# Performance work log

Measured on AMD Instinct MI355X. Metric: run time of the kernel, lower is better.

The kernel has to match this reference:

```python
import jax, jax.numpy as jnp
import numpy as np

D, U, H = 3, 256, 8
DH = U // H
B, N, E = 128, 128, 512
BN_SCALE = 1.0 / np.sqrt(1.0 + 1e-3)  # keras BatchNorm inference with init moving stats (mean=0, var=1)


def setup_inputs() -> dict:
    key = jax.random.key(0)
    k = jax.random.split(key, 16)
    p = lambda kk, sh: jax.random.normal(kk, sh, jnp.float32) * 0.05
    return {
        "node_attr": jax.random.normal(k[0], (B, N, U), jnp.float32),
        "edge_attr": jax.random.normal(k[1], (B, E, U), jnp.float32),
        "edge_indices": jax.random.randint(k[2], (B, E, 2), 0, N, dtype=jnp.int32),
        "W_edge": p(k[3], (D, 3 * U, U)), "b_edge": jnp.zeros((D, U)),
        "gamma_e": jnp.ones((D, U)), "beta_e": jnp.zeros((D, U)),
        "W_node": p(k[4], (D, U, U)), "b_node": jnp.zeros((D, U)),
        "gamma_n": jnp.ones((D, U)), "beta_n": jnp.zeros((D, U)),
        "W_gat": p(k[5], (D, U, H, DH)), "a_gat": p(k[6], (D, H, 2 * DH + U)), "b_gat": jnp.zeros((D, H)),
        "W_gru": p(k[7], (D, U, 3 * U)), "U_gru": p(k[8], (D, U, 3 * U)), "b_gru": jnp.zeros((D, 3 * U)),
        "W_p1": p(k[9], (U, U)), "b_p1": jnp.zeros((U,)),
        "W_p2": p(k[10], (U, U // 2)), "b_p2": jnp.zeros((U // 2,)),
    }


def _bn(x, gamma, beta):
    # inference batchnorm with moving_mean=0, moving_var=1
    return x * (gamma * BN_SCALE) + beta


def _gather(nodes, idx):
    # nodes [B,N,F], idx [B,E] -> [B,E,F]
    return jnp.take_along_axis(nodes, idx[..., None], axis=1)


def _gat_one(h, eidx, edge, a, b):
    # h [N,H,DH], eidx [E,2], edge [E,U]; aggregate messages from src (col 1) at tgt (col 0)
    tgt, src = eidx[:, 0], eidx[:, 1]
    hi, hj = h[tgt], h[src]
    logit = (jnp.einsum('ehd,hd->eh', hi, a[:, :DH])
             + jnp.einsum('ehd,hd->eh', hj, a[:, DH:2 * DH])
             + edge @ a[:, 2 * DH:].T + b)
    logit = jax.nn.leaky_relu(logit, 0.2)
    # per-target-node segment softmax over variable-degree neighborhoods
    m = jnp.full((N, H), -1e9, logit.dtype).at[tgt].max(logit)
    ex = jnp.exp(logit - m[tgt])
    den = jnp.zeros((N, H), logit.dtype).at[tgt].add(ex) + 1e-9
    att = ex / den[tgt]
    out = jnp.zeros((N, H, DH), h.dtype).at[tgt].add(att[..., None] * hj)
    return out.reshape(N, H * DH)


def reference(node_attr, edge_attr, edge_indices, W_edge, b_edge, gamma_e, beta_e,
              W_node, b_node, gamma_n, beta_n, W_gat, a_gat, b_gat,
              W_gru, U_gru, b_gru, W_p1, b_p1, W_p2, b_p2):
    nodes, edges = node_attr, edge_attr
    tgt_idx = edge_indices[..., 0]
    src_idx = edge_indices[..., 1]
    for d in range(D):
        # edge update: gather endpoints, concat with edge feats, MLP, graph batchnorm
        e_in = _gather(nodes, src_idx)   # GatherNodesOutgoing
        e_out = _gather(nodes, tgt_idx)  # GatherNodesIngoing
        ec = jnp.concatenate([e_in, e_out, edges], axis=-1)  # [B,E,3U]
        e_up = _bn(jax.nn.relu(ec @ W_edge[d] + b_edge[d]), gamma_e[d], beta_e[d])
        # multi-head GAT attention over edges
        h = jnp.einsum('bnf,fhd->bnhd', nodes, W_gat[d])
        attended = jax.nn.relu(jax.vmap(_gat_one, in_axes=(0, 0, 0, None, None))(
            h, edge_indices, e_up, a_gat[d], b_gat[d]))
        # node MLP + batchnorm
        n_up = _bn(jax.nn.relu(nodes @ W_node[d] + b_node[d]), gamma_n[d], beta_n[d])
        # GRU update: state = n_up, input = attended
        xp = attended @ W_gru[d] + b_gru[d]
        hp = n_up @ U_gru[d]
        z = jax.nn.sigmoid(xp[..., :U] + hp[..., :U])
        r = jax.nn.sigmoid(xp[..., U:2 * U] + hp[..., U:2 * U])
        hh = jnp.tanh(xp[..., 2 * U:] + r * hp[..., 2 * U:])
        nodes = z * n_up + (1.0 - z) * hh
        edges = e_up
    emb = jnp.mean(nodes, axis=1)
    emb = jax.nn.relu(emb @ W_p1 + b_p1)
    emb = jax.nn.relu(emb @ W_p2 + b_p2)
    # inference-mode view augmentation is identity, so both views equal the base embedding
    views = jnp.stack([emb, emb], axis=1)  # [B, num_views, U//2]
    return emb, views
```

## Files before the change

### kernel.cpp

```cpp
#include <hip/hip_runtime.h>
#include <hip/hip_bf16.h>

constexpr int Dn  = 3;
constexpr int Un  = 256;
constexpr int Hn  = 8;
constexpr int DHn = 32;
constexpr int Bn  = 128;
constexpr int Nn  = 128;
constexpr int En  = 512;
constexpr float BN_SCALE_C = 0.9995003746877732f;

#define LB __launch_bounds__(256)
#define LB8 __launch_bounds__(512)

typedef short bf16x8 __attribute__((ext_vector_type(8)));
typedef unsigned short u16x8 __attribute__((ext_vector_type(8)));
typedef float f32x4 __attribute__((ext_vector_type(4)));
#define MFMA16(a, b, c) __builtin_amdgcn_mfma_f32_16x16x32_bf16(a, b, c, 0, 0, 0)

__device__ __forceinline__ void gload16(const void* g, void* l) {
  __builtin_amdgcn_global_load_lds(
      (const __attribute__((address_space(1))) void*)g,
      (__attribute__((address_space(3))) void*)l, 16, 0, 0);
}
__device__ __forceinline__ float sigm(float x) { return 1.f / (1.f + expf(-x)); }
__device__ __forceinline__ float bf2f(unsigned short u) {
  return __uint_as_float((unsigned)u << 16);
}

__global__ LB void k_f2bf(const float* __restrict__ in,
                          __hip_bfloat16* __restrict__ out, int n) {
  int i = (blockIdx.x * 256 + threadIdx.x) * 4;
  if (i + 3 < n) {
    float4 v = *reinterpret_cast<const float4*>(in + i);
    out[i + 0] = __float2bfloat16(v.x);
    out[i + 1] = __float2bfloat16(v.y);
    out[i + 2] = __float2bfloat16(v.z);
    out[i + 3] = __float2bfloat16(v.w);
  }
}

__global__ LB void k_prep_edge(const float* __restrict__ W,
                               __hip_bfloat16* __restrict__ Wt) {
  int idx = blockIdx.x * 256 + threadIdx.x;
  int d = idx / (Un * 3 * Un);
  int rem = idx % (Un * 3 * Un);
  int n = rem / (3 * Un);
  int k = rem % (3 * Un);
  Wt[idx] = __float2bfloat16(W[(size_t)d * 3 * Un * Un + (size_t)k * Un + n]);
}

__global__ LB void k_prep_hn(const float* __restrict__ Wg,
                             const float* __restrict__ Wn,
                             __hip_bfloat16* __restrict__ Wt) {
  int idx = blockIdx.x * 256 + threadIdx.x;
  int d = idx / (512 * 256);
  int rem = idx % (512 * 256);
  int n = rem / 256;
  int k = rem % 256;
  float v = (n < 256) ? Wg[(size_t)d * 65536 + k * 256 + n]
                      : Wn[(size_t)d * 65536 + k * 256 + (n - 256)];
  Wt[idx] = __float2bfloat16(v);
}

__global__ LB void k_prep_gru2(const float* __restrict__ W,
                               const float* __restrict__ U,
                               __hip_bfloat16* __restrict__ Wt) {
  int idx = blockIdx.x * 256 + threadIdx.x;
  int d = idx / (768 * 512);
  int rem = idx % (768 * 512);
  int j2 = rem >> 9;
  int k = rem & 511;
  const size_t wb = (size_t)d * 196608;
  float v = (k < 256) ? W[wb + k * 768 + j2] : U[wb + (k - 256) * 768 + j2];
  Wt[idx] = __float2bfloat16(v);
}

__global__ LB8 void k_edge_mfma(const __hip_bfloat16* __restrict__ nodes,
                                const __hip_bfloat16* __restrict__ edges,
                                const int* __restrict__ eidx,
                                const __hip_bfloat16* __restrict__ Wt,
                                const float* __restrict__ bias,
                                const float* __restrict__ gamma,
                                const float* __restrict__ beta,
                                __hip_bfloat16* __restrict__ e_up) {
  __shared__ __align__(16) short As[128 * 64];
  __shared__ __align__(16) short Bs[256 * 64];
  const int tid = threadIdx.x, lane = tid & 63;
  const int w = tid >> 6, wr = w >> 2, wc = w & 3;
  const int bid = blockIdx.x;
  const int wgid = (bid & 7) * 64 + (bid >> 3);
  const int row0 = wgid * 128;
  const __hip_bfloat16 *pa0[2], *pa1[2], *pa2[2], *pb[4];
  int sxa[2], sxb[4];
#pragma unroll
  for (int i = 0; i < 2; ++i) {
    int c = i * 512 + tid, row = c >> 3, slot = c & 7;
    int R = row0 + row, b = R >> 9, e = R & 511;
    int tt = eidx[(b * En + e) * 2 + 0];
    int ss = eidx[(b * En + e) * 2 + 1];
    pa0[i] = nodes + (size_t)(b * Nn + ss) * Un;
    pa1[i] = nodes + (size_t)(b * Nn + tt) * Un;
    pa2[i] = edges + (size_t)(b * En + e) * Un;
    sxa[i] = (slot ^ (row & 7)) * 8;
  }
#pragma unroll
  for (int i = 0; i < 4; ++i) {
    int c = i * 512 + tid, j = c >> 3, slot = c & 7;
    pb[i] = Wt + (size_t)j * 768;
    sxb[i] = (slot ^ (j & 7)) * 8;
  }
  f32x4 acc[4][4] = {};
  const int ldsb = (tid & 448) * 16;
  for (int kt = 0; kt < 768; kt += 64) {
    const int region = kt >> 8, koff = kt & 255;
#pragma unroll
    for (int i = 0; i < 2; ++i) {
      const __hip_bfloat16* s = (region == 0) ? pa0[i] : (region == 1 ? pa1[i] : pa2[i]);
      gload16(s + koff + sxa[i], (char*)As + i * 8192 + ldsb);
    }
#pragma unroll
    for (int i = 0; i < 4; ++i)
      gload16(pb[i] + kt + sxb[i], (char*)Bs + i * 8192 + ldsb);
    __syncthreads();
#pragma unroll
    for (int ks = 0; ks < 2; ++ks) {
      const int lc = ks * 4 + (lane >> 4);
      bf16x8 af[4], bfv[4];
#pragma unroll
      for (int mi = 0; mi < 4; ++mi) {
        int row = wr * 64 + mi * 16 + (lane & 15);
        af[mi] = *(const bf16x8*)((const char*)As + row * 128 + ((lc ^ (row & 7)) << 4));
      }
#pragma unroll
      for (int ni = 0; ni < 4; ++ni) {
        int col = wc * 64 + ni * 16 + (lane & 15);
        bfv[ni] = *(const bf16x8*)((const char*)Bs + col * 128 + ((lc ^ (col & 7)) << 4));
      }
#pragma unroll
      for (int mi = 0; mi < 4; ++mi)
#pragma unroll
        for (int ni = 0; ni < 4; ++ni)
          acc[mi][ni] = MFMA16(af[mi], bfv[ni], acc[mi][ni]);
    }
    __syncthreads();
  }
#pragma unroll
  for (int mi = 0; mi < 4; ++mi)
#pragma unroll
    for (int ni = 0; ni < 4; ++ni) {
      int C = wc * 64 + ni * 16 + (lane & 15);
      float gs = gamma[C] * BN_SCALE_C, bt = beta[C], bi = bias[C];
#pragma unroll
      for (int r = 0; r < 4; ++r) {
        int R = row0 + wr * 64 + mi * 16 + (lane >> 4) * 4 + r;
        float v = acc[mi][ni][r] + bi;
        v = fmaxf(v, 0.f) * gs + bt;
        e_up[(size_t)R * Un + C] = __float2bfloat16(v);
      }
    }
}

__global__ LB8 void k_hn_mfma(const __hip_bfloat16* __restrict__ A,
                              const __hip_bfloat16* __restrict__ Wt,
                              const float* __restrict__ nb,
                              const float* __restrict__ ng,
                              const float* __restrict__ nbe,
                              __hip_bfloat16* __restrict__ h_bf,
                              __hip_bfloat16* __restrict__ nupb) {
  __shared__ __align__(16) short As[128 * 64];
  __shared__ __align__(16) short Bs[256 * 64];
  const int tid = threadIdx.x, lane = tid & 63;
  const int w = tid >> 6, wr = w >> 2, wc = w & 3;
  const int bid = blockIdx.x;
  const int wgid = (bid & 7) * 32 + (bid >> 3);
  const int row0 = (wgid >> 1) * 128, col0 = (wgid & 1) * 256;
  const __hip_bfloat16 *pa[2], *pb[4];
  int sxa[2], sxb[4];
#pragma unroll
  for (int i = 0; i < 2; ++i) {
    int c = i * 512 + tid, row = c >> 3, slot = c & 7;
    pa[i] = A + (size_t)(row0 + row) * Un;
    sxa[i] = (slot ^ (row & 7)) * 8;
  }
#pragma unroll
  for (int i = 0; i < 4; ++i) {
    int c = i * 512 + tid, j = c >> 3, slot = c & 7;
    pb[i] = Wt + (size_t)(col0 + j) * Un;
    sxb[i] = (slot ^ (j & 7)) * 8;
  }
  f32x4 acc[4][4] = {};
  const int ldsb = (tid & 448) * 16;
  for (int kt = 0; kt < 256; kt += 64) {
#pragma unroll
    for (int i = 0; i < 2; ++i)
      gload16(pa[i] + kt + sxa[i], (char*)As + i * 8192 + ldsb);
#pragma unroll
    for (int i = 0; i < 4; ++i)
      gload16(pb[i] + kt + sxb[i], (char*)Bs + i * 8192 + ldsb);
    __syncthreads();
#pragma unroll
    for (int ks = 0; ks < 2; ++ks) {
      const int lc = ks * 4 + (lane >> 4);
      bf16x8 af[4], bfv[4];
#pragma unroll
      for (int mi = 0; mi < 4; ++mi) {
        int row = wr * 64 + mi * 16 + (lane & 15);
        af[mi] = *(const bf16x8*)((const char*)As + row * 128 + ((lc ^ (row & 7)) << 4));
      }
#pragma unroll
      for (int ni = 0; ni < 4; ++ni) {
        int col = wc * 64 + ni * 16 + (lane & 15);
        bfv[ni] = *(const bf16x8*)((const char*)Bs + col * 128 + ((lc ^ (col & 7)) << 4));
      }
#pragma unroll
      for (int mi = 0; mi < 4; ++mi)
#pragma unroll
        for (int ni = 0; ni < 4; ++ni)
          acc[mi][ni] = MFMA16(af[mi], bfv[ni], acc[mi][ni]);
    }
    __syncthreads();
  }
  const bool is_h = (col0 < 256);
#pragma unroll
  for (int mi = 0; mi < 4; ++mi)
#pragma unroll
    for (int ni = 0; ni < 4; ++ni) {
      int c2 = wc * 64 + ni * 16 + (lane & 15);
#pragma unroll
      for (int r = 0; r < 4; ++r) {
        int R = row0 + wr * 64 + mi * 16 + (lane >> 4) * 4 + r;
        float v = acc[mi][ni][r];
        if (is_h) {
          h_bf[(size_t)R * Un + c2] = __float2bfloat16(v);
        } else {
          v += nb[c2];
          v = fmaxf(v, 0.f) * (ng[c2] * BN_SCALE_C) + nbe[c2];
          nupb[(size_t)R * Un + c2] = __float2bfloat16(v);
        }
      }
    }
}

__global__ LB8 void k_gru_mfma3(const __hip_bfloat16* __restrict__ attb,
                                const __hip_bfloat16* __restrict__ nupb,
                                const __hip_bfloat16* __restrict__ Wt,
                                const float* __restrict__ bg,
                                __hip_bfloat16* __restrict__ nodes_out) {
  __shared__ __align__(16) short As[128 * 64];
  __shared__ __align__(16) short Bs[192 * 64];
  const int tid = threadIdx.x, lane = tid & 63;
  const int w = tid >> 6, wr = w >> 2, wc = w & 3;
  const int bid = blockIdx.x;
  const int wgid = (bid & 7) * 64 + (bid >> 3);
  const int row0 = (wgid >> 2) * 128, c0 = (wgid & 3) * 64;
  const __hip_bfloat16 *paA[2], *paN[2], *pb[3];
  int sxa[2], sxb[3];
#pragma unroll
  for (int i = 0; i < 2; ++i) {
    int c = i * 512 + tid, row = c >> 3, slot = c & 7;
    paA[i] = attb + (size_t)(row0 + row) * Un;
    paN[i] = nupb + (size_t)(row0 + row) * Un;
    sxa[i] = (slot ^ (row & 7)) * 8;
  }
#pragma unroll
  for (int i = 0; i < 3; ++i) {
    int l = i * 512 + tid, j = l >> 3, slot = l & 7;
    int sec = j >> 6, jj = j & 63;
    pb[i] = Wt + (size_t)(sec * 256 + c0 + jj) * 512;
    sxb[i] = (slot ^ (j & 7)) * 8;
  }
  f32x4 acc[4][4] = {};
  const int ldsb = (tid & 448) * 16;
  for (int kt = 0; kt < 512; kt += 64) {
    const int koff = kt & 255;
    const bool rA = kt < 256;
#pragma unroll
    for (int i = 0; i < 2; ++i) {
      const __hip_bfloat16* s = rA ? paA[i] : paN[i];
      gload16(s + koff + sxa[i], (char*)As + i * 8192 + ldsb);
    }
#pragma unroll
    for (int i = 0; i < 3; ++i)
      gload16(pb[i] + kt + sxb[i], (char*)Bs + i * 8192 + ldsb);
    __syncthreads();
    const int g2 = rA ? 2 : 3;
#pragma unroll
    for (int ks = 0; ks < 2; ++ks) {
      const int lc = ks * 4 + (lane >> 4);
      bf16x8 af[4], bv[3];
#pragma unroll
      for (int s = 0; s < 3; ++s) {
        int j = s * 64 + wc * 16 + (lane & 15);
        bv[s] = *(const bf16x8*)((const char*)Bs + j * 128 + ((lc ^ (j & 7)) << 4));
      }
#pragma unroll
      for (int mi = 0; mi < 4; ++mi) {
        int row = wr * 64 + mi * 16 + (lane & 15);
        af[mi] = *(const bf16x8*)((const char*)As + row * 128 + ((lc ^ (row & 7)) << 4));
      }
#pragma unroll
      for (int mi = 0; mi < 4; ++mi) {
        acc[0][mi] = MFMA16(af[mi], bv[0], acc[0][mi]);
        acc[1][mi] = MFMA16(af[mi], bv[1], acc[1][mi]);
        acc[g2][mi] = MFMA16(af[mi], bv[2], acc[g2][mi]);
      }
    }
    __syncthreads();
  }
  {
    const int c = c0 + wc * 16 + (lane & 15);
    const float bz = bg[c], br = bg[256 + c], bh = bg[512 + c];
    const unsigned short* nu_u = (const unsigned short*)nupb;
#pragma unroll
    for (int mi = 0; mi < 4; ++mi)
#pragma unroll
      for (int r = 0; r < 4; ++r) {
        int R = row0 + wr * 64 + mi * 16 + (lane >> 4) * 4 + r;
        float z  = sigm(acc[0][mi][r] + bz);
        float rr = sigm(acc[1][mi][r] + br);
        float hh = tanhf(acc[2][mi][r] + bh + rr * acc[3][mi][r]);
        float nu = bf2f(nu_u[(size_t)R * Un + c]);
        nodes_out[(size_t)R * Un + c] = __float2bfloat16(z * nu + (1.f - z) * hh);
      }
  }
}

__global__ LB void k_elog_mfma(const __hip_bfloat16* __restrict__ e_up,
                               const float* __restrict__ a_gat,
                               float* __restrict__ elog) {
  __shared__ __align__(16) short at[16 * 264];
  const int tid = threadIdx.x, lane = tid & 63, w = tid >> 6;
  for (int l = tid; l < 16 * 264; l += 256) {
    int col = l / 264, k = l % 264;
    float v = (col < 8 && k < 256) ? a_gat[col * 320 + 64 + k] : 0.f;
    __hip_bfloat16 b = __float2bfloat16(v);
    at[l] = *reinterpret_cast<short*>(&b);
  }
  __syncthreads();
  const int rowbase = blockIdx.x * 256 + w * 64;
  const int lrow = lane & 15, lk = (lane >> 4) * 8;
  f32x4 acc[4] = {};
#pragma unroll
  for (int kt = 0; kt < 256; kt += 32) {
    bf16x8 bf = *(const bf16x8*)(at + lrow * 264 + kt + lk);
#pragma unroll
    for (int mi = 0; mi < 4; ++mi) {
      bf16x8 af = *(const bf16x8*)(e_up + (size_t)(rowbase + mi * 16 + lrow) * 256 + kt + lk);
      acc[mi] = MFMA16(af, bf, acc[mi]);
    }
  }
  if (lrow < 8) {
#pragma unroll
    for (int mi = 0; mi < 4; ++mi)
#pragma unroll
      for (int r = 0; r < 4; ++r) {
        int row = rowbase + mi * 16 + (lane >> 4) * 4 + r;
        elog[(size_t)row * 8 + lrow] = acc[mi][r];
      }
  }
}

__global__ LB void k_gat4(const __hip_bfloat16* __restrict__ h,
                          const float* __restrict__ elog,
                          const int* __restrict__ eidx,
                          const float* __restrict__ a_gat,
                          const float* __restrict__ b_gat,
                          __hip_bfloat16* __restrict__ att_bf) {
  const int b = blockIdx.x, q = blockIdx.y;
  __shared__ int s_tgt[En], s_src[En];
  __shared__ float s_at[32], s_as[32];
  __shared__ float s_lt[Nn], s_ls[Nn];
  __shared__ float s_L[En];
  __shared__ int s_cnt[Nn], s_start[Nn], s_cur[Nn];
  __shared__ short s_ord[En];
  __shared__ __align__(16) unsigned short hl[Nn][40];
  const int tid = threadIdx.x;
  const float bgq = b_gat[q];
  if (tid < 32) {
    s_at[tid] = a_gat[q * 320 + tid];
    s_as[tid] = a_gat[q * 320 + 32 + tid];
  }
  for (int e = tid; e < En; e += 256) {
    s_tgt[e] = eidx[(b * En + e) * 2 + 0];
    s_src[e] = eidx[(b * En + e) * 2 + 1];
  }
  if (tid < Nn) s_cnt[tid] = 0;
  for (int e = tid; e < En; e += 256)
    s_L[e] = elog[(size_t)(b * En + e) * 8 + q];
  const unsigned short* hu = (const unsigned short*)h;
  for (int l = tid; l < Nn * 4; l += 256) {
    int row = l >> 2, c8 = l & 3;
    u16x8 v = *(const u16x8*)(hu + (size_t)(b * Nn + row) * Un + q * DHn + c8 * 8);
    *(u16x8*)&hl[row][c8 * 8] = v;
  }
  __syncthreads();
  if (tid < Nn) {
    const unsigned short* hr = hl[tid];
    float lt = 0.f, ls = 0.f;
#pragma unroll
    for (int c8 = 0; c8 < 4; ++c8) {
      u16x8 v = *(const u16x8*)(hr + c8 * 8);
#pragma unroll
      for (int j = 0; j < 8; ++j) {
        float f = bf2f(v[j]);
        int d = c8 * 8 + j;
        lt += f * s_at[d];
        ls += f * s_as[d];
      }
    }
    s_lt[tid] = lt; s_ls[tid] = ls;
  }
  for (int e = tid; e < En; e += 256) atomicAdd(&s_cnt[s_tgt[e]], 1);
  __syncthreads();
  if (tid == 0) {
    int acc = 0;
    for (int n = 0; n < Nn; ++n) { s_start[n] = acc; s_cur[n] = acc; acc += s_cnt[n]; }
  }
  __syncthreads();
  for (int e = tid; e < En; e += 256) {
    int pos = atomicAdd(&s_cur[s_tgt[e]], 1);
    s_ord[pos] = (short)e;
  }
  for (int e = tid; e < En; e += 256) {
    float v = s_lt[s_tgt[e]] + s_ls[s_src[e]] + s_L[e] + bgq;
    v = (v > 0.f) ? v : 0.2f * v;
    s_L[e] = v;
  }
  __syncthreads();
  if (tid < Nn) {
    const int st = s_start[tid], cn = s_cnt[tid];
    float m = -1e9f;
    for (int i = 0; i < cn; ++i) m = fmaxf(m, s_L[s_ord[st + i]]);
    float den = 1e-9f;
    for (int i = 0; i < cn; ++i) {
      const int e = s_ord[st + i];
      float ex = expf(s_L[e] - m);
      s_L[e] = ex;
      den += ex;
    }
    s_lt[tid] = 1.f / den;
  }
  __syncthreads();
  {
    const int n = tid >> 1, half = tid & 1;
    const int st = s_start[n], cn = s_cnt[n];
    const float inv = s_lt[n];
    float acc[16] = {};
    for (int i = 0; i < cn; ++i) {
      const int e = s_ord[st + i];
      const float wgt = s_L[e] * inv;
      const unsigned short* hs = &hl[s_src[e]][half * 16];
#pragma unroll
      for (int c8 = 0; c8 < 2; ++c8) {
        u16x8 v = *(const u16x8*)(hs + c8 * 8);
#pragma unroll
        for (int j = 0; j < 8; ++j) acc[c8 * 8 + j] += wgt * bf2f(v[j]);
      }
    }
    __hip_bfloat16* ob = att_bf + (size_t)(b * Nn + n) * Un + q * DHn + half * 16;
#pragma unroll
    for (int d = 0; d < 16; ++d) ob[d] = __float2bfloat16(fmaxf(acc[d], 0.f));
  }
}

__global__ LB void k_pool(const __hip_bfloat16* __restrict__ nodes,
                          const float* __restrict__ Wp1, const float* __restrict__ bp1,
                          const float* __restrict__ Wp2, const float* __restrict__ bp2,
                          float* __restrict__ out) {
  const int b = blockIdx.x, tid = threadIdx.x;
  __shared__ float e0[256], e1[256];
  float s = 0.f;
  for (int n = 0; n < Nn; ++n) s += __bfloat162float(nodes[(size_t)(b * Nn + n) * Un + tid]);
  e0[tid] = s * (1.f / Nn);
  __syncthreads();
  float a1 = bp1[tid];
  for (int k = 0; k < 256; ++k) a1 += e0[k] * Wp1[k * 256 + tid];
  e1[tid] = fmaxf(a1, 0.f);
  __syncthreads();
  if (tid < 128) {
    float a2 = bp2[tid];
    for (int k = 0; k < 256; ++k) a2 += e1[k] * Wp2[k * 128 + tid];
    a2 = fmaxf(a2, 0.f);
    out[b * 128 + tid] = a2;
    out[Bn * 128 + b * 256 + tid] = a2;
    out[Bn * 128 + b * 256 + 128 + tid] = a2;
  }
}

extern "C" void kernel_launch(void* const* d_in, const int* in_sizes, int n_in,
                              void* d_out, int out_size, void* d_ws, size_t ws_size,
                              hipStream_t stream) {
  const float* node_attr = (const float*)d_in[0];
  const float* edge_attr = (const float*)d_in[1];
  const int*   eidx      = (const int*)d_in[2];
  const float* W_edge    = (const float*)d_in[3];
  const float* b_edge    = (const float*)d_in[4];
  const float* gamma_e   = (const float*)d_in[5];
  const float* beta_e    = (const float*)d_in[6];
  const float* W_node    = (const float*)d_in[7];
  const float* b_node    = (const float*)d_in[8];
  const float* gamma_n   = (const float*)d_in[9];
  const float* beta_n    = (const float*)d_in[10];
  const float* W_gat     = (const float*)d_in[11];
  const float* a_gat     = (const float*)d_in[12];
  const float* b_gat     = (const float*)d_in[13];
  const float* W_gru     = (const float*)d_in[14];
  const float* U_gru     = (const float*)d_in[15];
  const float* b_gru     = (const float*)d_in[16];
  const float* W_p1      = (const float*)d_in[17];
  const float* b_p1      = (const float*)d_in[18];
  const float* W_p2      = (const float*)d_in[19];
  const float* b_p2      = (const float*)d_in[20];

  char* p = (char*)d_ws;
  auto alloc = [&](size_t bytes) { char* q = p; p += (bytes + 255) & ~255ull; return q; };
  const size_t NODE_EL = (size_t)Bn * Nn * Un;
  const size_t EDGE_EL = (size_t)Bn * En * Un;
  __hip_bfloat16* nodes_bf = (__hip_bfloat16*)alloc(NODE_EL * 2);
  __hip_bfloat16* h_bf   = (__hip_bfloat16*)alloc(NODE_EL * 2);
  __hip_bfloat16* nup_bf = (__hip_bfloat16*)alloc(NODE_EL * 2);
  __hip_bfloat16* att_bf = (__hip_bfloat16*)alloc(NODE_EL * 2);
  float* elog   = (float*)alloc((size_t)Bn * En * 8 * 4);
  __hip_bfloat16* edges_a = (__hip_bfloat16*)alloc(EDGE_EL * 2);
  __hip_bfloat16* edges_b = (__hip_bfloat16*)alloc(EDGE_EL * 2);
  __hip_bfloat16* Wt_e   = (__hip_bfloat16*)alloc((size_t)Dn * 256 * 768 * 2);
  __hip_bfloat16* Wt_hn  = (__hip_bfloat16*)alloc((size_t)Dn * 512 * 256 * 2);
  __hip_bfloat16* Wt_gru = (__hip_bfloat16*)alloc((size_t)Dn * 768 * 512 * 2);

  k_f2bf<<<(int)(EDGE_EL / 1024), 256, 0, stream>>>(edge_attr, edges_a, (int)EDGE_EL);
  k_f2bf<<<(int)(NODE_EL / 1024), 256, 0, stream>>>(node_attr, nodes_bf, (int)NODE_EL);
  k_prep_edge<<<(Dn * 256 * 768) / 256, 256, 0, stream>>>(W_edge, Wt_e);
  k_prep_hn<<<(Dn * 512 * 256) / 256, 256, 0, stream>>>(W_gat, W_node, Wt_hn);
  k_prep_gru2<<<(Dn * 768 * 512) / 256, 256, 0, stream>>>(W_gru, U_gru, Wt_gru);

  __hip_bfloat16* ein = edges_a;
  __hip_bfloat16* eout = edges_b;
  for (int d = 0; d < Dn; ++d) {
    k_edge_mfma<<<512, 512, 0, stream>>>(
        nodes_bf, ein, eidx, Wt_e + (size_t)d * 256 * 768, b_edge + d * Un,
        gamma_e + d * Un, beta_e + d * Un, eout);
    k_hn_mfma<<<256, 512, 0, stream>>>(
        nodes_bf, Wt_hn + (size_t)d * 512 * 256, b_node + d * Un,
        gamma_n + d * Un, beta_n + d * Un, h_bf, nup_bf);
    k_elog_mfma<<<(Bn * En) / 256, 256, 0, stream>>>(
        eout, a_gat + (size_t)d * Hn * 320, elog);
    k_gat4<<<dim3(Bn, Hn), 256, 0, stream>>>(
        h_bf, elog, eidx, a_gat + (size_t)d * Hn * 320, b_gat + d * Hn, att_bf);
    k_gru_mfma3<<<512, 512, 0, stream>>>(
        att_bf, nup_bf, Wt_gru + (size_t)d * 768 * 512, b_gru + d * 3 * Un,
        nodes_bf);
    __hip_bfloat16* t = ein; ein = eout; eout = t;
  }
  k_pool<<<Bn, 256, 0, stream>>>(nodes_bf, W_p1, b_p1, W_p2, b_p2, (float*)d_out);
}
```

Before: 366.6 us.

## Double-buffer LDS tiles with BK=32 in edge and GRU MFMA GEMMs

Switches the edge-MLP and GRU GEMM kernels from a single 64-wide K tile to double-buffered 32-wide K tiles. The next tile's global-to-LDS load is issued before computing on the current one, cutting one barrier per iteration and aiming to overlap memory latency with MFMA work. The XOR swizzle is adapted to 4 slots per row. The trade-off is twice as many loop iterations with half the MFMA work each, and the swizzle on 64-byte rows may cause more LDS bank conflicts.

```diff
diff --git a/kernel.cpp b/kernel.cpp
--- a/kernel.cpp
+++ b/kernel.cpp
@@ -84,66 +84,68 @@
                                 const float* __restrict__ gamma,
                                 const float* __restrict__ beta,
                                 __hip_bfloat16* __restrict__ e_up) {
-  __shared__ __align__(16) short As[128 * 64];
-  __shared__ __align__(16) short Bs[256 * 64];
+  __shared__ __align__(16) short As[2][128 * 32];
+  __shared__ __align__(16) short Bs[2][256 * 32];
   const int tid = threadIdx.x, lane = tid & 63;
   const int w = tid >> 6, wr = w >> 2, wc = w & 3;
   const int bid = blockIdx.x;
   const int wgid = (bid & 7) * 64 + (bid >> 3);
   const int row0 = wgid * 128;
-  const __hip_bfloat16 *pa0[2], *pa1[2], *pa2[2], *pb[4];
-  int sxa[2], sxb[4];
-#pragma unroll
-  for (int i = 0; i < 2; ++i) {
-    int c = i * 512 + tid, row = c >> 3, slot = c & 7;
+  const __hip_bfloat16 *pa0, *pa1, *pa2;
+  int sxa;
+  {
+    int row = tid >> 2, slot = tid & 3;
     int R = row0 + row, b = R >> 9, e = R & 511;
     int tt = eidx[(b * En + e) * 2 + 0];
     int ss = eidx[(b * En + e) * 2 + 1];
-    pa0[i] = nodes + (size_t)(b * Nn + ss) * Un;
-    pa1[i] = nodes + (size_t)(b * Nn + tt) * Un;
-    pa2[i] = edges + (size_t)(b * En + e) * Un;
-    sxa[i] = (slot ^ (row & 7)) * 8;
-  }
-#pragma unroll
-  for (int i = 0; i < 4; ++i) {
-    int c = i * 512 + tid, j = c >> 3, slot = c & 7;
+    pa0 = nodes + (size_t)(b * Nn + ss) * Un;
+    pa1 = nodes + (size_t)(b * Nn + tt) * Un;
+    pa2 = edges + (size_t)(b * En + e) * Un;
+    sxa = (slot ^ (row & 3)) * 8;
+  }
+  const __hip_bfloat16* pb[2];
+  int sxb[2];
+#pragma unroll
+  for (int i = 0; i < 2; ++i) {
+    int c = i * 512 + tid, j = c >> 2, slot = c & 3;
     pb[i] = Wt + (size_t)j * 768;
-    sxb[i] = (slot ^ (j & 7)) * 8;
+    sxb[i] = (slot ^ (j & 3)) * 8;
   }
   f32x4 acc[4][4] = {};
   const int ldsb = (tid & 448) * 16;
-  for (int kt = 0; kt < 768; kt += 64) {
+
+  auto stage = [&](int buf, int kt) {
     const int region = kt >> 8, koff = kt & 255;
-#pragma unroll
-    for (int i = 0; i < 2; ++i) {
-      const __hip_bfloat16* s = (region == 0) ? pa0[i] : (region == 1 ? pa1[i] : pa2[i]);
-      gload16(s + koff + sxa[i], (char*)As + i * 8192 + ldsb);
-    }
-#pragma unroll
-    for (int i = 0; i < 4; ++i)
-      gload16(pb[i] + kt + sxb[i], (char*)Bs + i * 8192 + ldsb);
+    const __hip_bfloat16* s = (region == 0) ? pa0 : (region == 1 ? pa1 : pa2);
+    gload16(s + koff + sxa, (char*)As[buf] + ldsb);
+    gload16(pb[0] + kt + sxb[0], (char*)Bs[buf] + ldsb);
+    gload16(pb[1] + kt + sxb[1], (char*)Bs[buf] + 8192 + ldsb);
+  };
+
+  stage(0, 0);
+  __syncthreads();
+  int cur = 0;
+  const int lc = lane >> 4;
+  for (int kt = 0; kt < 768; kt += 32) {
+    if (kt + 32 < 768) stage(cur ^ 1, kt + 32);
+    bf16x8 af[4], bfv[4];
+#pragma unroll
+    for (int mi = 0; mi < 4; ++mi) {
+      int row = wr * 64 + mi * 16 + (lane & 15);
+      af[mi] = *(const bf16x8*)((const char*)As[cur] + row * 64 + ((lc ^ (row & 3)) << 4));
+    }
+#pragma unroll
+    for (int ni = 0; ni < 4; ++ni) {
+      int col = wc * 64 + ni * 16 + (lane & 15);
+      bfv[ni] = *(const bf16x8*)((const char*)Bs[cur] + col * 64 + ((lc ^ (col & 3)) << 4));
+    }
+#pragma unroll
+    for (int mi = 0; mi < 4; ++mi)
+#pragma unroll
+      for (int ni = 0; ni < 4; ++ni)
+        acc[mi][ni] = MFMA16(af[mi], bfv[ni], acc[mi][ni]);
     __syncthreads();
-#pragma unroll
-    for (int ks = 0; ks < 2; ++ks) {
-      const int lc = ks * 4 + (lane >> 4);
-      bf16x8 af[4], bfv[4];
-#pragma unroll
-      for (int mi = 0; mi < 4; ++mi) {
-        int row = wr * 64 + mi * 16 + (lane & 15);
-        af[mi] = *(const bf16x8*)((const char*)As + row * 128 + ((lc ^ (row & 7)) << 4));
-      }
-#pragma unroll
-      for (int ni = 0; ni < 4; ++ni) {
-        int col = wc * 64 + ni * 16 + (lane & 15);
-        bfv[ni] = *(const bf16x8*)((const char*)Bs + col * 128 + ((lc ^ (col & 7)) << 4));
-      }
-#pragma unroll
-      for (int mi = 0; mi < 4; ++mi)
-#pragma unroll
-        for (int ni = 0; ni < 4; ++ni)
-          acc[mi][ni] = MFMA16(af[mi], bfv[ni], acc[mi][ni]);
-    }
-    __syncthreads();
+    cur ^= 1;
   }
 #pragma unroll
   for (int mi = 0; mi < 4; ++mi)
@@ -242,71 +244,74 @@
     }
 }
 
-__global__ LB8 void k_gru_mfma3(const __hip_bfloat16* __restrict__ attb,
+__global__ LB8 void k_gru_mfma4(const __hip_bfloat16* __restrict__ attb,
                                 const __hip_bfloat16* __restrict__ nupb,
                                 const __hip_bfloat16* __restrict__ Wt,
                                 const float* __restrict__ bg,
                                 __hip_bfloat16* __restrict__ nodes_out) {
-  __shared__ __align__(16) short As[128 * 64];
-  __shared__ __align__(16) short Bs[192 * 64];
+  __shared__ __align__(16) short As[2][128 * 32];
+  __shared__ __align__(16) short Bs[2][192 * 32];
   const int tid = threadIdx.x, lane = tid & 63;
   const int w = tid >> 6, wr = w >> 2, wc = w & 3;
   const int bid = blockIdx.x;
   const int wgid = (bid & 7) * 64 + (bid >> 3);
   const int row0 = (wgid >> 2) * 128, c0 = (wgid & 3) * 64;
-  const __hip_bfloat16 *paA[2], *paN[2], *pb[3];
-  int sxa[2], sxb[3];
-#pragma unroll
-  for (int i = 0; i < 2; ++i) {
-    int c = i * 512 + tid, row = c >> 3, slot = c & 7;
-    paA[i] = attb + (size_t)(row0 + row) * Un;
-    paN[i] = nupb + (size_t)(row0 + row) * Un;
-    sxa[i] = (slot ^ (row & 7)) * 8;
-  }
-#pragma unroll
-  for (int i = 0; i < 3; ++i) {
-    int l = i * 512 + tid, j = l >> 3, slot = l & 7;
+  const __hip_bfloat16 *paA, *paN, *pb0, *pb1;
+  int sxa, sxb0, sxb1;
+  {
+    int row = tid >> 2, slot = tid & 3;
+    paA = attb + (size_t)(row0 + row) * Un;
+    paN = nupb + (size_t)(row0 + row) * Un;
+    sxa = (slot ^ (row & 3)) * 8;
+  }
+  {
+    int j = tid >> 2, slot = tid & 3;
     int sec = j >> 6, jj = j & 63;
-    pb[i] = Wt + (size_t)(sec * 256 + c0 + jj) * 512;
-    sxb[i] = (slot ^ (j & 7)) * 8;
+    pb0 = Wt + (size_t)(sec * 256 + c0 + jj) * 512;
+    sxb0 = (slot ^ (j & 3)) * 8;
+    int c = 512 + tid, j1 = c >> 2, s1 = c & 3;
+    int jj1 = j1 & 63;
+    pb1 = Wt + (size_t)(2 * 256 + c0 + jj1) * 512;
+    sxb1 = (s1 ^ (j1 & 3)) * 8;
   }
   f32x4 acc[4][4] = {};
   const int ldsb = (tid & 448) * 16;
-  for (int kt = 0; kt < 512; kt += 64) {
+  const bool doB1 = (tid < 256);
+
+  auto stage = [&](int buf, int kt) {
     const int koff = kt & 255;
-    const bool rA = kt < 256;
-#pragma unroll
-    for (int i = 0; i < 2; ++i) {
-      const __hip_bfloat16* s = rA ? paA[i] : paN[i];
-      gload16(s + koff + sxa[i], (char*)As + i * 8192 + ldsb);
-    }
-#pragma unroll
-    for (int i = 0; i < 3; ++i)
-      gload16(pb[i] + kt + sxb[i], (char*)Bs + i * 8192 + ldsb);
+    const __hip_bfloat16* s = (kt < 256) ? paA : paN;
+    gload16(s + koff + sxa, (char*)As[buf] + ldsb);
+    gload16(pb0 + kt + sxb0, (char*)Bs[buf] + ldsb);
+    if (doB1) gload16(pb1 + kt + sxb1, (char*)Bs[buf] + 8192 + ldsb);
+  };
+
+  stage(0, 0);
+  __syncthreads();
+  int cur = 0;
+  const int lc = lane >> 4;
+  for (int kt = 0; kt < 512; kt += 32) {
+    if (kt + 32 < 512) stage(cur ^ 1, kt + 32);
+    const int g2 = (kt < 256) ? 2 : 3;
+    bf16x8 af[4], bv[3];
+#pragma unroll
+    for (int s = 0; s < 3; ++s) {
+      int j = s * 64 + wc * 16 + (lane & 15);
+      bv[s] = *(const bf16x8*)((const char*)Bs[cur] + j * 64 + ((lc ^ (j & 3)) << 4));
+    }
+#pragma unroll
+    for (int mi = 0; mi < 4; ++mi) {
+      int row = wr * 64 + mi * 16 + (lane & 15);
+      af[mi] = *(const bf16x8*)((const char*)As[cur] + row * 64 + ((lc ^ (row & 3)) << 4));
+    }
+#pragma unroll
+    for (int mi = 0; mi < 4; ++mi) {
+      acc[0][mi] = MFMA16(af[mi], bv[0], acc[0][mi]);
+      acc[1][mi] = MFMA16(af[mi], bv[1], acc[1][mi]);
+      acc[g2][mi] = MFMA16(af[mi], bv[2], acc[g2][mi]);
+    }
     __syncthreads();
-    const int g2 = rA ? 2 : 3;
-#pragma unroll
-    for (int ks = 0; ks < 2; ++ks) {
-      const int lc = ks * 4 + (lane >> 4);
-      bf16x8 af[4], bv[3];
-#pragma unroll
-      for (int s = 0; s < 3; ++s) {
-        int j = s * 64 + wc * 16 + (lane & 15);
-        bv[s] = *(const bf16x8*)((const char*)Bs + j * 128 + ((lc ^ (j & 7)) << 4));
-      }
-#pragma unroll
-      for (int mi = 0; mi < 4; ++mi) {
-        int row = wr * 64 + mi * 16 + (lane & 15);
-        af[mi] = *(const bf16x8*)((const char*)As + row * 128 + ((lc ^ (row & 7)) << 4));
-      }
-#pragma unroll
-      for (int mi = 0; mi < 4; ++mi) {
-        acc[0][mi] = MFMA16(af[mi], bv[0], acc[0][mi]);
-        acc[1][mi] = MFMA16(af[mi], bv[1], acc[1][mi]);
-        acc[g2][mi] = MFMA16(af[mi], bv[2], acc[g2][mi]);
-      }
-    }
-    __syncthreads();
+    cur ^= 1;
   }
   {
     const int c = c0 + wc * 16 + (lane & 15);
@@ -547,7 +552,7 @@
         eout, a_gat + (size_t)d * Hn * 320, elog);
     k_gat4<<<dim3(Bn, Hn), 256, 0, stream>>>(
         h_bf, elog, eidx, a_gat + (size_t)d * Hn * 320, b_gat + d * Hn, att_bf);
-    k_gru_mfma3<<<512, 512, 0, stream>>>(
+    k_gru_mfma4<<<512, 512, 0, stream>>>(
         att_bf, nup_bf, Wt_gru + (size_t)d * 768 * 512, b_gru + d * 3 * Un,
         nodes_bf);
     __hip_bfloat16* t = ein; ein = eout; eout = t;
```

Result: slower. 392.0 us (+6.9%).
